# Kernel tuning notes

Hardware: AMD Instinct MI355X
Metric: run time of the kernel (lower is better)

Reference implementation:

```python
import jax, jax.numpy as jnp
import numpy as np

B, T, C, H, L, NC = 4096, 400, 42, 16, 2, 2  # batch, seq_len, input_size, hidden, layers, classes


def setup_inputs() -> dict:
    key = jax.random.key(0)
    ks = jax.random.split(key, 12)
    k = 1.0 / np.sqrt(H)  # torch nn.RNN uniform(-1/sqrt(H), 1/sqrt(H)) init scale
    u = lambda kk, shape: jax.random.uniform(kk, shape, jnp.float32, -k, k)
    return {
        "x": jax.random.normal(ks[0], (B, C * T), jnp.float32),
        "h0": jnp.zeros((L, B, H), jnp.float32),
        "W_ih0": u(ks[1], (H, C)),
        "W_hh0": u(ks[2], (H, H)),
        "b_ih0": u(ks[3], (H,)),
        "b_hh0": u(ks[4], (H,)),
        "W_ih1": u(ks[5], (H, H)),
        "W_hh1": u(ks[6], (H, H)),
        "b_ih1": u(ks[7], (H,)),
        "b_hh1": u(ks[8], (H,)),
        "W_fc": jax.random.normal(ks[9], (NC, H), jnp.float32) * np.sqrt(2.0 / H),  # kaiming_normal_
        "b_fc": u(ks[10], (NC,)),
    }


def _rnn_layer(seq, h, W_ih, W_hh, b_ih, b_hh):
    # seq: (B, T, F); vanilla tanh RNN, batch_first. Returns full output sequence (B, T, H).
    bias = b_ih + b_hh

    def step(h, xt):  # xt: (B, F), h: (B, H)
        h = jnp.tanh(xt @ W_ih.T + h @ W_hh.T + bias)
        return h, h

    _, ys = jax.lax.scan(step, h, seq.transpose(1, 0, 2))  # ys: (T, B, H)
    return ys.transpose(1, 0, 2)


def reference(x, h0, W_ih0, W_hh0, b_ih0, b_hh0, W_ih1, W_hh1, b_ih1, b_hh1, W_fc, b_fc):
    # x.view(B, -1, 400).transpose(2, 1) -> (B, T=400, C=42)
    xs = x.reshape(B, C, T).transpose(0, 2, 1)
    y0 = _rnn_layer(xs, h0[0], W_ih0, W_hh0, b_ih0, b_hh0)  # (B, T, H)
    y1 = _rnn_layer(y0, h0[1], W_ih1, W_hh1, b_ih1, b_hh1)  # (B, T, H)
    h_t = y1[:, -1, :]  # last timestep of top layer
    return h_t @ W_fc.T + b_fc  # (B, NC)
```

## Files before the change

kernel.cpp:

```cpp
#include <hip/hip_runtime.h>
#include <hip/hip_fp16.h>

#define NB 4096
#define NT 400
#define NCH 42
#define NH 16
#define NT4 100

#define RORI(v,K) __builtin_amdgcn_update_dpp(0, (v), 0x120+(K), 0xF, 0xF, true)
#define RORF(v,K) __int_as_float(__builtin_amdgcn_update_dpp(0, __float_as_int(v), 0x120+(K), 0xF, 0xF, true))

static __device__ __forceinline__ float fast_tanh(float x) {
  float ax = __builtin_fabsf(x);
  float e  = __expf(2.0f * ax);
  float r  = __builtin_fmaf(-2.0f, __builtin_amdgcn_rcpf(e + 1.0f), 1.0f);
  return __builtin_copysignf(r, x);
}

static __device__ __forceinline__ uint pack_h2(float a, float b) {
  __half ha = __float2half(a), hb = __float2half(b);
  return (uint)__half_as_ushort(ha) | ((uint)__half_as_ushort(hb) << 16);
}

__global__ __launch_bounds__(128) void proj0_kernel(
    const float* __restrict__ x, const float* __restrict__ Wih0,
    const float* __restrict__ bih0, const float* __restrict__ bhh0,
    uint4* __restrict__ P)
{
  __shared__ float Wl[NH * NCH];
  __shared__ float bl[NH];
  const int tid = threadIdx.x;
  for (int i = tid; i < NH * NCH; i += 128) Wl[i] = Wih0[i];
  if (tid < NH) bl[tid] = bih0[tid] + bhh0[tid];
  __syncthreads();

  const int b  = blockIdx.x;
  const int t4 = tid;
  if (t4 >= NT4) return;

  float4 acc[NH];
#pragma unroll
  for (int j = 0; j < NH; ++j) { float bb = bl[j]; acc[j] = make_float4(bb, bb, bb, bb); }

  const float* xrow = x + (size_t)b * (NCH * NT) + t4 * 4;
#pragma unroll
  for (int cc = 0; cc < NCH; cc += 7) {
    float4 xv[7];
#pragma unroll
    for (int u = 0; u < 7; ++u) xv[u] = *(const float4*)(xrow + (size_t)(cc + u) * NT);
#pragma unroll
    for (int u = 0; u < 7; ++u) {
#pragma unroll
      for (int j = 0; j < NH; ++j) {
        float w = Wl[j * NCH + cc + u];
        acc[j].x = __builtin_fmaf(xv[u].x, w, acc[j].x);
        acc[j].y = __builtin_fmaf(xv[u].y, w, acc[j].y);
        acc[j].z = __builtin_fmaf(xv[u].z, w, acc[j].z);
        acc[j].w = __builtin_fmaf(xv[u].w, w, acc[j].w);
      }
    }
  }

  uint4* Pout = P + ((size_t)t4 * NB + b) * 8;
#pragma unroll
  for (int jp = 0; jp < 8; ++jp) {
    const float4 a0 = acc[2 * jp], a1 = acc[2 * jp + 1];
    uint4 ov;
    ov.x = pack_h2(a0.x, a0.y);
    ov.y = pack_h2(a0.z, a0.w);
    ov.z = pack_h2(a1.x, a1.y);
    ov.w = pack_h2(a1.z, a1.w);
    Pout[jp] = ov;
  }
}

__global__ __launch_bounds__(256) void rnn_seq_kernel(
    const uint2* __restrict__ P, const float* __restrict__ h0in,
    const float* __restrict__ Whh0, const float* __restrict__ Wih1,
    const float* __restrict__ Whh1, const float* __restrict__ bih1,
    const float* __restrict__ bhh1, const float* __restrict__ Wfc,
    const float* __restrict__ bfc, float* __restrict__ out)
{
  const int gtid = blockIdx.x * blockDim.x + threadIdx.x;
  const int b = gtid >> 4;
  const int j = threadIdx.x & 15;

  float w0[NH], wi1[NH], wh1[NH];
  w0[0]  = Whh0[j * NH + j];
  wi1[0] = Wih1[j * NH + j];
  wh1[0] = Whh1[j * NH + j];
#define LOADW(K) { int sj = RORI(j, K) & 15; \
  w0[K]  = Whh0[j * NH + sj]; \
  wi1[K] = Wih1[j * NH + sj]; \
  wh1[K] = Whh1[j * NH + sj]; }
  LOADW(1) LOADW(2) LOADW(3) LOADW(4) LOADW(5) LOADW(6) LOADW(7) LOADW(8)
  LOADW(9) LOADW(10) LOADW(11) LOADW(12) LOADW(13) LOADW(14) LOADW(15)
#undef LOADW
  const float b1   = bih1[j] + bhh1[j];
  const float wfc0 = Wfc[j];
  const float wfc1 = Wfc[NH + j];

  float h0 = h0in[b * NH + j];
  float h1 = h0in[(size_t)NB * NH + b * NH + j];

  const size_t pstride = (size_t)NB * NH;
  const size_t pidx    = (size_t)b * NH + j;
  uint2 pc = P[pidx];
  uint2 pn = P[pidx + pstride];

  for (int t4 = 0; t4 < NT4; ++t4) {
    const int nx = (t4 + 2 < NT4) ? (t4 + 2) : (NT4 - 1);
    uint2 p2 = P[pidx + (size_t)nx * pstride];

    union { uint2 u; __half2 h[2]; } cv; cv.u = pc;
    float2 f0 = __half22float2(cv.h[0]);
    float2 f1 = __half22float2(cv.h[1]);
    float pv[4] = {f0.x, f0.y, f1.x, f1.y};

#pragma unroll
    for (int q = 0; q < 4; ++q) {
      float a  = __builtin_fmaf(h0, w0[0], pv[q]);
      float a2 = 0.0f;
#define L0T(K) { float hv = RORF(h0, K); \
  if ((K) & 1) a2 = __builtin_fmaf(hv, w0[K], a2); \
  else         a  = __builtin_fmaf(hv, w0[K], a); }
      L0T(1) L0T(2) L0T(3) L0T(4) L0T(5) L0T(6) L0T(7) L0T(8)
      L0T(9) L0T(10) L0T(11) L0T(12) L0T(13) L0T(14) L0T(15)
#undef L0T
      float h0n = fast_tanh(a + a2);

      float c1 = __builtin_fmaf(h0n, wi1[0], b1);
      float c2 = h1 * wh1[0];
#define L1A(K) { float hv = RORF(h0n, K); \
  if ((K) & 1) c2 = __builtin_fmaf(hv, wi1[K], c2); \
  else         c1 = __builtin_fmaf(hv, wi1[K], c1); }
      L1A(1) L1A(2) L1A(3) L1A(4) L1A(5) L1A(6) L1A(7) L1A(8)
      L1A(9) L1A(10) L1A(11) L1A(12) L1A(13) L1A(14) L1A(15)
#undef L1A
#define L1B(K) { float hv = RORF(h1, K); \
  if ((K) & 1) c1 = __builtin_fmaf(hv, wh1[K], c1); \
  else         c2 = __builtin_fmaf(hv, wh1[K], c2); }
      L1B(1) L1B(2) L1B(3) L1B(4) L1B(5) L1B(6) L1B(7) L1B(8)
      L1B(9) L1B(10) L1B(11) L1B(12) L1B(13) L1B(14) L1B(15)
#undef L1B
      h1 = fast_tanh(c1 + c2);
      h0 = h0n;
    }
    pc = pn;
    pn = p2;
  }

  float v0 = h1 * wfc0;
  float v1 = h1 * wfc1;
#pragma unroll
  for (int m = 8; m >= 1; m >>= 1) {
    v0 += __shfl_xor(v0, m, 16);
    v1 += __shfl_xor(v1, m, 16);
  }
  if (j == 0) {
    float* o = out + (size_t)b * 2;
    o[0] = v0 + bfc[0];
    o[1] = v1 + bfc[1];
  }
}

extern "C" void kernel_launch(void* const* d_in, const int* in_sizes, int n_in,
                              void* d_out, int out_size, void* d_ws, size_t ws_size,
                              hipStream_t stream) {
  const float* x    = (const float*)d_in[0];
  const float* h0   = (const float*)d_in[1];
  const float* Wih0 = (const float*)d_in[2];
  const float* Whh0 = (const float*)d_in[3];
  const float* bih0 = (const float*)d_in[4];
  const float* bhh0 = (const float*)d_in[5];
  const float* Wih1 = (const float*)d_in[6];
  const float* Whh1 = (const float*)d_in[7];
  const float* bih1 = (const float*)d_in[8];
  const float* bhh1 = (const float*)d_in[9];
  const float* Wfc  = (const float*)d_in[10];
  const float* bfc  = (const float*)d_in[11];
  float* outp = (float*)d_out;

  proj0_kernel<<<NB, 128, 0, stream>>>(x, Wih0, bih0, bhh0, (uint4*)d_ws);
  rnn_seq_kernel<<<(NB * NH) / 256, 256, 0, stream>>>(
      (const uint2*)d_ws, h0, Whh0, Wih1, Whh1, bih1, bhh1, Wfc, bfc, outp);
}
```

Before: 550.8 us.

## Process two batch rows per thread group in RNN and split projection hidden dims

The recurrent kernel now has each 16-lane group advance two independent batch sequences in interleaved fashion. This gives the scheduler two independent dependency chains to hide DPP and FMA latency, and halves the grid to 128 blocks. The projection kernel splits the 16 hidden outputs across two thread halves using a transposed, vector-loadable weight layout in shared memory, which halves accumulator registers. The cost is fewer resident waves in the RNN kernel: 128 blocks on a 256-CU part leaves many CUs idle, while each wave gets more ILP.

```diff
diff --git a/kernel.cpp b/kernel.cpp
--- a/kernel.cpp
+++ b/kernel.cpp
@@ -22,27 +22,31 @@
   return (uint)__half_as_ushort(ha) | ((uint)__half_as_ushort(hb) << 16);
 }
 
-__global__ __launch_bounds__(128) void proj0_kernel(
+__global__ __launch_bounds__(256) void proj0_kernel(
     const float* __restrict__ x, const float* __restrict__ Wih0,
     const float* __restrict__ bih0, const float* __restrict__ bhh0,
     uint4* __restrict__ P)
 {
-  __shared__ float Wl[NH * NCH];
+  __shared__ float WlT[NCH * NH];
   __shared__ float bl[NH];
   const int tid = threadIdx.x;
-  for (int i = tid; i < NH * NCH; i += 128) Wl[i] = Wih0[i];
+  for (int i = tid; i < NCH * NH; i += 256)
+    WlT[i] = Wih0[(i & 15) * NCH + (i >> 4)];
   if (tid < NH) bl[tid] = bih0[tid] + bhh0[tid];
   __syncthreads();
 
   const int b  = blockIdx.x;
-  const int t4 = tid;
+  const int jh = tid >> 7;
+  const int t4 = tid & 127;
   if (t4 >= NT4) return;
 
-  float4 acc[NH];
-#pragma unroll
-  for (int j = 0; j < NH; ++j) { float bb = bl[j]; acc[j] = make_float4(bb, bb, bb, bb); }
-
-  const float* xrow = x + (size_t)b * (NCH * NT) + t4 * 4;
+  float4 acc[8];
+#pragma unroll
+  for (int jj = 0; jj < 8; ++jj) { float bb = bl[jh * 8 + jj]; acc[jj] = make_float4(bb, bb, bb, bb); }
+
+  const float*  xrow = x + (size_t)b * (NCH * NT) + t4 * 4;
+  const float4* WT4  = (const float4*)WlT;
+
 #pragma unroll
   for (int cc = 0; cc < NCH; cc += 7) {
     float4 xv[7];
@@ -50,27 +54,30 @@
     for (int u = 0; u < 7; ++u) xv[u] = *(const float4*)(xrow + (size_t)(cc + u) * NT);
 #pragma unroll
     for (int u = 0; u < 7; ++u) {
-#pragma unroll
-      for (int j = 0; j < NH; ++j) {
-        float w = Wl[j * NCH + cc + u];
-        acc[j].x = __builtin_fmaf(xv[u].x, w, acc[j].x);
-        acc[j].y = __builtin_fmaf(xv[u].y, w, acc[j].y);
-        acc[j].z = __builtin_fmaf(xv[u].z, w, acc[j].z);
-        acc[j].w = __builtin_fmaf(xv[u].w, w, acc[j].w);
+      const int c = cc + u;
+      float4 wA = WT4[c * 4 + jh * 2];
+      float4 wB = WT4[c * 4 + jh * 2 + 1];
+      float wv[8] = {wA.x, wA.y, wA.z, wA.w, wB.x, wB.y, wB.z, wB.w};
+#pragma unroll
+      for (int jj = 0; jj < 8; ++jj) {
+        acc[jj].x = __builtin_fmaf(xv[u].x, wv[jj], acc[jj].x);
+        acc[jj].y = __builtin_fmaf(xv[u].y, wv[jj], acc[jj].y);
+        acc[jj].z = __builtin_fmaf(xv[u].z, wv[jj], acc[jj].z);
+        acc[jj].w = __builtin_fmaf(xv[u].w, wv[jj], acc[jj].w);
       }
     }
   }
 
-  uint4* Pout = P + ((size_t)t4 * NB + b) * 8;
-#pragma unroll
-  for (int jp = 0; jp < 8; ++jp) {
-    const float4 a0 = acc[2 * jp], a1 = acc[2 * jp + 1];
+  uint4* Pout = P + ((size_t)t4 * NB + b) * 8 + jh * 4;
+#pragma unroll
+  for (int k = 0; k < 4; ++k) {
+    const float4 a0 = acc[2 * k], a1 = acc[2 * k + 1];
     uint4 ov;
     ov.x = pack_h2(a0.x, a0.y);
     ov.y = pack_h2(a0.z, a0.w);
     ov.z = pack_h2(a1.x, a1.y);
     ov.w = pack_h2(a1.z, a1.w);
-    Pout[jp] = ov;
+    Pout[k] = ov;
   }
 }
 
@@ -82,8 +89,9 @@
     const float* __restrict__ bfc, float* __restrict__ out)
 {
   const int gtid = blockIdx.x * blockDim.x + threadIdx.x;
-  const int b = gtid >> 4;
+  const int g = gtid >> 4;
   const int j = threadIdx.x & 15;
+  const int b0 = g, bS = g + (NB / 2);
 
   float w0[NH], wi1[NH], wh1[NH];
   w0[0]  = Whh0[j * NH + j];
@@ -96,71 +104,85 @@
   LOADW(1) LOADW(2) LOADW(3) LOADW(4) LOADW(5) LOADW(6) LOADW(7) LOADW(8)
   LOADW(9) LOADW(10) LOADW(11) LOADW(12) LOADW(13) LOADW(14) LOADW(15)
 #undef LOADW
-  const float b1   = bih1[j] + bhh1[j];
+  const float b1c  = bih1[j] + bhh1[j];
   const float wfc0 = Wfc[j];
   const float wfc1 = Wfc[NH + j];
 
-  float h0 = h0in[b * NH + j];
-  float h1 = h0in[(size_t)NB * NH + b * NH + j];
-
-  const size_t pstride = (size_t)NB * NH;
-  const size_t pidx    = (size_t)b * NH + j;
-  uint2 pc = P[pidx];
-  uint2 pn = P[pidx + pstride];
+  float h0A = h0in[b0 * NH + j];
+  float h1A = h0in[(size_t)NB * NH + b0 * NH + j];
+  float h0B = h0in[bS * NH + j];
+  float h1B = h0in[(size_t)NB * NH + bS * NH + j];
+
+  const size_t ps = (size_t)NB * NH;
+  const size_t iA = (size_t)b0 * NH + j;
+  const size_t iB = (size_t)bS * NH + j;
+  uint2 cA = P[iA],      cB = P[iB];
+  uint2 nA = P[iA + ps], nB = P[iB + ps];
 
   for (int t4 = 0; t4 < NT4; ++t4) {
     const int nx = (t4 + 2 < NT4) ? (t4 + 2) : (NT4 - 1);
-    uint2 p2 = P[pidx + (size_t)nx * pstride];
-
-    union { uint2 u; __half2 h[2]; } cv; cv.u = pc;
-    float2 f0 = __half22float2(cv.h[0]);
-    float2 f1 = __half22float2(cv.h[1]);
-    float pv[4] = {f0.x, f0.y, f1.x, f1.y};
+    uint2 fA = P[iA + (size_t)nx * ps];
+    uint2 fB = P[iB + (size_t)nx * ps];
+
+    union { uint2 u; __half2 h[2]; } uA, uB;
+    uA.u = cA; uB.u = cB;
+    float2 a01 = __half22float2(uA.h[0]), a23 = __half22float2(uA.h[1]);
+    float2 b01 = __half22float2(uB.h[0]), b23 = __half22float2(uB.h[1]);
+    float pvA[4] = {a01.x, a01.y, a23.x, a23.y};
+    float pvB[4] = {b01.x, b01.y, b23.x, b23.y};
 
 #pragma unroll
     for (int q = 0; q < 4; ++q) {
-      float a  = __builtin_fmaf(h0, w0[0], pv[q]);
-      float a2 = 0.0f;
-#define L0T(K) { float hv = RORF(h0, K); \
-  if ((K) & 1) a2 = __builtin_fmaf(hv, w0[K], a2); \
-  else         a  = __builtin_fmaf(hv, w0[K], a); }
+      float aA = __builtin_fmaf(h0A, w0[0], pvA[q]), a2A = 0.0f;
+      float aB = __builtin_fmaf(h0B, w0[0], pvB[q]), a2B = 0.0f;
+#define L0T(K) { float hvA = RORF(h0A, K); float hvB = RORF(h0B, K); \
+  if ((K) & 1) { a2A = __builtin_fmaf(hvA, w0[K], a2A); a2B = __builtin_fmaf(hvB, w0[K], a2B); } \
+  else         { aA  = __builtin_fmaf(hvA, w0[K], aA);  aB  = __builtin_fmaf(hvB, w0[K], aB);  } }
       L0T(1) L0T(2) L0T(3) L0T(4) L0T(5) L0T(6) L0T(7) L0T(8)
       L0T(9) L0T(10) L0T(11) L0T(12) L0T(13) L0T(14) L0T(15)
 #undef L0T
-      float h0n = fast_tanh(a + a2);
-
-      float c1 = __builtin_fmaf(h0n, wi1[0], b1);
-      float c2 = h1 * wh1[0];
-#define L1A(K) { float hv = RORF(h0n, K); \
-  if ((K) & 1) c2 = __builtin_fmaf(hv, wi1[K], c2); \
-  else         c1 = __builtin_fmaf(hv, wi1[K], c1); }
+      float h0nA = fast_tanh(aA + a2A);
+      float h0nB = fast_tanh(aB + a2B);
+
+      float c1A = __builtin_fmaf(h0nA, wi1[0], b1c), c2A = h1A * wh1[0];
+      float c1B = __builtin_fmaf(h0nB, wi1[0], b1c), c2B = h1B * wh1[0];
+#define L1A(K) { float hvA = RORF(h0nA, K); float hvB = RORF(h0nB, K); \
+  if ((K) & 1) { c2A = __builtin_fmaf(hvA, wi1[K], c2A); c2B = __builtin_fmaf(hvB, wi1[K], c2B); } \
+  else         { c1A = __builtin_fmaf(hvA, wi1[K], c1A); c1B = __builtin_fmaf(hvB, wi1[K], c1B); } }
       L1A(1) L1A(2) L1A(3) L1A(4) L1A(5) L1A(6) L1A(7) L1A(8)
       L1A(9) L1A(10) L1A(11) L1A(12) L1A(13) L1A(14) L1A(15)
 #undef L1A
-#define L1B(K) { float hv = RORF(h1, K); \
-  if ((K) & 1) c1 = __builtin_fmaf(hv, wh1[K], c1); \
-  else         c2 = __builtin_fmaf(hv, wh1[K], c2); }
+#define L1B(K) { float hvA = RORF(h1A, K); float hvB = RORF(h1B, K); \
+  if ((K) & 1) { c1A = __builtin_fmaf(hvA, wh1[K], c1A); c1B = __builtin_fmaf(hvB, wh1[K], c1B); } \
+  else         { c2A = __builtin_fmaf(hvA, wh1[K], c2A); c2B = __builtin_fmaf(hvB, wh1[K], c2B); } }
       L1B(1) L1B(2) L1B(3) L1B(4) L1B(5) L1B(6) L1B(7) L1B(8)
       L1B(9) L1B(10) L1B(11) L1B(12) L1B(13) L1B(14) L1B(15)
 #undef L1B
-      h1 = fast_tanh(c1 + c2);
-      h0 = h0n;
+      h1A = fast_tanh(c1A + c2A);
+      h1B = fast_tanh(c1B + c2B);
+      h0A = h0nA;
+      h0B = h0nB;
     }
-    pc = pn;
-    pn = p2;
-  }
-
-  float v0 = h1 * wfc0;
-  float v1 = h1 * wfc1;
+    cA = nA; cB = nB;
+    nA = fA; nB = fB;
+  }
+
+  float v0A = h1A * wfc0, v1A = h1A * wfc1;
+  float v0B = h1B * wfc0, v1B = h1B * wfc1;
 #pragma unroll
   for (int m = 8; m >= 1; m >>= 1) {
-    v0 += __shfl_xor(v0, m, 16);
-    v1 += __shfl_xor(v1, m, 16);
+    v0A += __shfl_xor(v0A, m, 16);
+    v1A += __shfl_xor(v1A, m, 16);
+    v0B += __shfl_xor(v0B, m, 16);
+    v1B += __shfl_xor(v1B, m, 16);
   }
   if (j == 0) {
-    float* o = out + (size_t)b * 2;
-    o[0] = v0 + bfc[0];
-    o[1] = v1 + bfc[1];
+    float* oA = out + (size_t)b0 * 2;
+    float* oB = out + (size_t)bS * 2;
+    oA[0] = v0A + bfc[0];
+    oA[1] = v1A + bfc[1];
+    oB[0] = v0B + bfc[0];
+    oB[1] = v1B + bfc[1];
   }
 }
 
@@ -181,7 +203,7 @@
   const float* bfc  = (const float*)d_in[11];
   float* outp = (float*)d_out;
 
-  proj0_kernel<<<NB, 128, 0, stream>>>(x, Wih0, bih0, bhh0, (uint4*)d_ws);
-  rnn_seq_kernel<<<(NB * NH) / 256, 256, 0, stream>>>(
+  proj0_kernel<<<NB, 256, 0, stream>>>(x, Wih0, bih0, bhh0, (uint4*)d_ws);
+  rnn_seq_kernel<<<(NB / 2 * NH) / 256, 256, 0, stream>>>(
       (const uint2*)d_ws, h0, Whh0, Wih1, Whh1, bih1, bhh1, Wfc, bfc, outp);
 }
```

Result: no change. 543.8 us (-1.3%).

## Split RNN layers across two wavefronts pipelined through LDS, retune projection

Applied to the files above, without the earlier changes.

The recurrent kernel now gives each 128-thread block two wavefronts. Wave 0 runs layer 0 and writes its hidden state to a double-buffered LDS slot, while wave 1 runs layer 1 one step behind. A __syncthreads at every timestep keeps the two in step. This shortens each wave's serial dependency chain but adds a block barrier per step and leaves half the threads inactive in each role. The projection kernel splits the 16 output features across two half-blocks using a transposed weight layout in LDS, and tanh drops its abs/copysign, which can overflow to NaN/inf behaviour for large negative inputs (exp→0 gives -1, fine; large positive gives inf, rcp→0, fine).

```diff
diff --git a/kernel.cpp b/kernel.cpp
--- a/kernel.cpp
+++ b/kernel.cpp
@@ -11,10 +11,8 @@
 #define RORF(v,K) __int_as_float(__builtin_amdgcn_update_dpp(0, __float_as_int(v), 0x120+(K), 0xF, 0xF, true))
 
 static __device__ __forceinline__ float fast_tanh(float x) {
-  float ax = __builtin_fabsf(x);
-  float e  = __expf(2.0f * ax);
-  float r  = __builtin_fmaf(-2.0f, __builtin_amdgcn_rcpf(e + 1.0f), 1.0f);
-  return __builtin_copysignf(r, x);
+  float e = __expf(2.0f * x);
+  return __builtin_fmaf(-2.0f, __builtin_amdgcn_rcpf(e + 1.0f), 1.0f);
 }
 
 static __device__ __forceinline__ uint pack_h2(float a, float b) {
@@ -22,27 +20,31 @@
   return (uint)__half_as_ushort(ha) | ((uint)__half_as_ushort(hb) << 16);
 }
 
-__global__ __launch_bounds__(128) void proj0_kernel(
+__global__ __launch_bounds__(256) void proj0_kernel(
     const float* __restrict__ x, const float* __restrict__ Wih0,
     const float* __restrict__ bih0, const float* __restrict__ bhh0,
     uint4* __restrict__ P)
 {
-  __shared__ float Wl[NH * NCH];
+  __shared__ float WlT[NCH * NH];
   __shared__ float bl[NH];
   const int tid = threadIdx.x;
-  for (int i = tid; i < NH * NCH; i += 128) Wl[i] = Wih0[i];
+  for (int i = tid; i < NCH * NH; i += 256)
+    WlT[i] = Wih0[(i & 15) * NCH + (i >> 4)];
   if (tid < NH) bl[tid] = bih0[tid] + bhh0[tid];
   __syncthreads();
 
   const int b  = blockIdx.x;
-  const int t4 = tid;
+  const int jh = tid >> 7;
+  const int t4 = tid & 127;
   if (t4 >= NT4) return;
 
-  float4 acc[NH];
-#pragma unroll
-  for (int j = 0; j < NH; ++j) { float bb = bl[j]; acc[j] = make_float4(bb, bb, bb, bb); }
-
-  const float* xrow = x + (size_t)b * (NCH * NT) + t4 * 4;
+  float4 acc[8];
+#pragma unroll
+  for (int jj = 0; jj < 8; ++jj) { float bb = bl[jh * 8 + jj]; acc[jj] = make_float4(bb, bb, bb, bb); }
+
+  const float*  xrow = x + (size_t)b * (NCH * NT) + t4 * 4;
+  const float4* WT4  = (const float4*)WlT;
+
 #pragma unroll
   for (int cc = 0; cc < NCH; cc += 7) {
     float4 xv[7];
@@ -50,40 +52,46 @@
     for (int u = 0; u < 7; ++u) xv[u] = *(const float4*)(xrow + (size_t)(cc + u) * NT);
 #pragma unroll
     for (int u = 0; u < 7; ++u) {
-#pragma unroll
-      for (int j = 0; j < NH; ++j) {
-        float w = Wl[j * NCH + cc + u];
-        acc[j].x = __builtin_fmaf(xv[u].x, w, acc[j].x);
-        acc[j].y = __builtin_fmaf(xv[u].y, w, acc[j].y);
-        acc[j].z = __builtin_fmaf(xv[u].z, w, acc[j].z);
-        acc[j].w = __builtin_fmaf(xv[u].w, w, acc[j].w);
+      const int c = cc + u;
+      float4 wA = WT4[c * 4 + jh * 2];
+      float4 wB = WT4[c * 4 + jh * 2 + 1];
+      float wv[8] = {wA.x, wA.y, wA.z, wA.w, wB.x, wB.y, wB.z, wB.w};
+#pragma unroll
+      for (int jj = 0; jj < 8; ++jj) {
+        acc[jj].x = __builtin_fmaf(xv[u].x, wv[jj], acc[jj].x);
+        acc[jj].y = __builtin_fmaf(xv[u].y, wv[jj], acc[jj].y);
+        acc[jj].z = __builtin_fmaf(xv[u].z, wv[jj], acc[jj].z);
+        acc[jj].w = __builtin_fmaf(xv[u].w, wv[jj], acc[jj].w);
       }
     }
   }
 
-  uint4* Pout = P + ((size_t)t4 * NB + b) * 8;
-#pragma unroll
-  for (int jp = 0; jp < 8; ++jp) {
-    const float4 a0 = acc[2 * jp], a1 = acc[2 * jp + 1];
+  uint4* Pout = P + ((size_t)t4 * NB + b) * 8 + jh * 4;
+#pragma unroll
+  for (int k = 0; k < 4; ++k) {
+    const float4 a0 = acc[2 * k], a1 = acc[2 * k + 1];
     uint4 ov;
     ov.x = pack_h2(a0.x, a0.y);
     ov.y = pack_h2(a0.z, a0.w);
     ov.z = pack_h2(a1.x, a1.y);
     ov.w = pack_h2(a1.z, a1.w);
-    Pout[jp] = ov;
-  }
-}
-
-__global__ __launch_bounds__(256) void rnn_seq_kernel(
+    Pout[k] = ov;
+  }
+}
+
+__global__ __launch_bounds__(128) void rnn_seq_kernel(
     const uint2* __restrict__ P, const float* __restrict__ h0in,
     const float* __restrict__ Whh0, const float* __restrict__ Wih1,
     const float* __restrict__ Whh1, const float* __restrict__ bih1,
     const float* __restrict__ bhh1, const float* __restrict__ Wfc,
     const float* __restrict__ bfc, float* __restrict__ out)
 {
-  const int gtid = blockIdx.x * blockDim.x + threadIdx.x;
-  const int b = gtid >> 4;
-  const int j = threadIdx.x & 15;
+  __shared__ float h0buf[2 * 64];
+  const int wid  = threadIdx.x >> 6;
+  const int lane = threadIdx.x & 63;
+  const int grp  = lane >> 4;
+  const int j    = lane & 15;
+  const int b    = blockIdx.x * 4 + grp;
 
   float w0[NH], wi1[NH], wh1[NH];
   w0[0]  = Whh0[j * NH + j];
@@ -96,71 +104,101 @@
   LOADW(1) LOADW(2) LOADW(3) LOADW(4) LOADW(5) LOADW(6) LOADW(7) LOADW(8)
   LOADW(9) LOADW(10) LOADW(11) LOADW(12) LOADW(13) LOADW(14) LOADW(15)
 #undef LOADW
-  const float b1   = bih1[j] + bhh1[j];
+  const float b1c  = bih1[j] + bhh1[j];
   const float wfc0 = Wfc[j];
   const float wfc1 = Wfc[NH + j];
 
   float h0 = h0in[b * NH + j];
   float h1 = h0in[(size_t)NB * NH + b * NH + j];
 
-  const size_t pstride = (size_t)NB * NH;
-  const size_t pidx    = (size_t)b * NH + j;
-  uint2 pc = P[pidx];
-  uint2 pn = P[pidx + pstride];
+  const size_t ps   = (size_t)NB * NH;
+  const size_t pidx = (size_t)b * NH + j;
+  uint2 pc, pn;
+  if (wid == 0) { pc = P[pidx]; pn = P[pidx + ps]; }
 
   for (int t4 = 0; t4 < NT4; ++t4) {
-    const int nx = (t4 + 2 < NT4) ? (t4 + 2) : (NT4 - 1);
-    uint2 p2 = P[pidx + (size_t)nx * pstride];
-
-    union { uint2 u; __half2 h[2]; } cv; cv.u = pc;
-    float2 f0 = __half22float2(cv.h[0]);
-    float2 f1 = __half22float2(cv.h[1]);
-    float pv[4] = {f0.x, f0.y, f1.x, f1.y};
+    uint2 p2;
+    float pv[4];
+    if (wid == 0) {
+      const int nx = (t4 + 2 < NT4) ? (t4 + 2) : (NT4 - 1);
+      p2 = P[pidx + (size_t)nx * ps];
+      union { uint2 u; __half2 h[2]; } cv; cv.u = pc;
+      float2 f0 = __half22float2(cv.h[0]);
+      float2 f1 = __half22float2(cv.h[1]);
+      pv[0] = f0.x; pv[1] = f0.y; pv[2] = f1.x; pv[3] = f1.y;
+    }
 
 #pragma unroll
     for (int q = 0; q < 4; ++q) {
-      float a  = __builtin_fmaf(h0, w0[0], pv[q]);
-      float a2 = 0.0f;
+      if (wid == 0) {
+        float a1 = __builtin_fmaf(h0, w0[0], pv[q]);
+        float a2 = 0.0f, a3 = 0.0f;
 #define L0T(K) { float hv = RORF(h0, K); \
-  if ((K) & 1) a2 = __builtin_fmaf(hv, w0[K], a2); \
-  else         a  = __builtin_fmaf(hv, w0[K], a); }
-      L0T(1) L0T(2) L0T(3) L0T(4) L0T(5) L0T(6) L0T(7) L0T(8)
-      L0T(9) L0T(10) L0T(11) L0T(12) L0T(13) L0T(14) L0T(15)
+  if      ((K) % 3 == 0) a1 = __builtin_fmaf(hv, w0[K], a1); \
+  else if ((K) % 3 == 1) a2 = __builtin_fmaf(hv, w0[K], a2); \
+  else                   a3 = __builtin_fmaf(hv, w0[K], a3); }
+        L0T(1) L0T(2) L0T(3) L0T(4) L0T(5) L0T(6) L0T(7) L0T(8)
+        L0T(9) L0T(10) L0T(11) L0T(12) L0T(13) L0T(14) L0T(15)
 #undef L0T
-      float h0n = fast_tanh(a + a2);
-
-      float c1 = __builtin_fmaf(h0n, wi1[0], b1);
-      float c2 = h1 * wh1[0];
-#define L1A(K) { float hv = RORF(h0n, K); \
-  if ((K) & 1) c2 = __builtin_fmaf(hv, wi1[K], c2); \
-  else         c1 = __builtin_fmaf(hv, wi1[K], c1); }
-      L1A(1) L1A(2) L1A(3) L1A(4) L1A(5) L1A(6) L1A(7) L1A(8)
-      L1A(9) L1A(10) L1A(11) L1A(12) L1A(13) L1A(14) L1A(15)
+        h0 = fast_tanh(a1 + (a2 + a3));
+        h0buf[(q & 1) * 64 + lane] = h0;
+      } else {
+        if (t4 > 0 || q > 0) {
+          float hp = h0buf[((q + 1) & 1) * 64 + lane];
+          float c2 = h1 * wh1[0];
+          float c3 = 0.0f;
+          float c1 = __builtin_fmaf(hp, wi1[0], b1c);
+#define L1B(K) { float hv = RORF(h1, K); \
+  if ((K) & 1) c2 = __builtin_fmaf(hv, wh1[K], c2); \
+  else         c3 = __builtin_fmaf(hv, wh1[K], c3); }
+          L1B(1) L1B(2) L1B(3) L1B(4) L1B(5) L1B(6) L1B(7) L1B(8)
+          L1B(9) L1B(10) L1B(11) L1B(12) L1B(13) L1B(14) L1B(15)
+#undef L1B
+#define L1A(K) { float hv = RORF(hp, K); \
+  if ((K) & 1) c1 = __builtin_fmaf(hv, wi1[K], c1); \
+  else         c3 = __builtin_fmaf(hv, wi1[K], c3); }
+          L1A(1) L1A(2) L1A(3) L1A(4) L1A(5) L1A(6) L1A(7) L1A(8)
+          L1A(9) L1A(10) L1A(11) L1A(12) L1A(13) L1A(14) L1A(15)
 #undef L1A
+          h1 = fast_tanh((c1 + c2) + c3);
+        }
+      }
+      __syncthreads();
+    }
+    if (wid == 0) { pc = pn; pn = p2; }
+  }
+
+  if (wid == 1) {
+    float hp = h0buf[1 * 64 + lane];
+    float c2 = h1 * wh1[0];
+    float c3 = 0.0f;
+    float c1 = __builtin_fmaf(hp, wi1[0], b1c);
 #define L1B(K) { float hv = RORF(h1, K); \
-  if ((K) & 1) c1 = __builtin_fmaf(hv, wh1[K], c1); \
-  else         c2 = __builtin_fmaf(hv, wh1[K], c2); }
-      L1B(1) L1B(2) L1B(3) L1B(4) L1B(5) L1B(6) L1B(7) L1B(8)
-      L1B(9) L1B(10) L1B(11) L1B(12) L1B(13) L1B(14) L1B(15)
+  if ((K) & 1) c2 = __builtin_fmaf(hv, wh1[K], c2); \
+  else         c3 = __builtin_fmaf(hv, wh1[K], c3); }
+    L1B(1) L1B(2) L1B(3) L1B(4) L1B(5) L1B(6) L1B(7) L1B(8)
+    L1B(9) L1B(10) L1B(11) L1B(12) L1B(13) L1B(14) L1B(15)
 #undef L1B
-      h1 = fast_tanh(c1 + c2);
-      h0 = h0n;
-    }
-    pc = pn;
-    pn = p2;
-  }
-
-  float v0 = h1 * wfc0;
-  float v1 = h1 * wfc1;
-#pragma unroll
-  for (int m = 8; m >= 1; m >>= 1) {
-    v0 += __shfl_xor(v0, m, 16);
-    v1 += __shfl_xor(v1, m, 16);
-  }
-  if (j == 0) {
-    float* o = out + (size_t)b * 2;
-    o[0] = v0 + bfc[0];
-    o[1] = v1 + bfc[1];
+#define L1A(K) { float hv = RORF(hp, K); \
+  if ((K) & 1) c1 = __builtin_fmaf(hv, wi1[K], c1); \
+  else         c3 = __builtin_fmaf(hv, wi1[K], c3); }
+    L1A(1) L1A(2) L1A(3) L1A(4) L1A(5) L1A(6) L1A(7) L1A(8)
+    L1A(9) L1A(10) L1A(11) L1A(12) L1A(13) L1A(14) L1A(15)
+#undef L1A
+    h1 = fast_tanh((c1 + c2) + c3);
+
+    float v0 = h1 * wfc0;
+    float v1 = h1 * wfc1;
+#pragma unroll
+    for (int m = 8; m >= 1; m >>= 1) {
+      v0 += __shfl_xor(v0, m, 16);
+      v1 += __shfl_xor(v1, m, 16);
+    }
+    if (j == 0) {
+      float* o = out + (size_t)b * 2;
+      o[0] = v0 + bfc[0];
+      o[1] = v1 + bfc[1];
+    }
   }
 }
 
@@ -181,7 +219,7 @@
   const float* bfc  = (const float*)d_in[11];
   float* outp = (float*)d_out;
 
-  proj0_kernel<<<NB, 128, 0, stream>>>(x, Wih0, bih0, bhh0, (uint4*)d_ws);
-  rnn_seq_kernel<<<(NB * NH) / 256, 256, 0, stream>>>(
+  proj0_kernel<<<NB, 256, 0, stream>>>(x, Wih0, bih0, bhh0, (uint4*)d_ws);
+  rnn_seq_kernel<<<NB / 4, 128, 0, stream>>>(
       (const uint2*)d_ws, h0, Whh0, Wih1, Whh1, bih1, bhh1, Wfc, bfc, outp);
 }
```

Result: faster. 539.4 us (-2.1%).
